# Kernel tuning notes

Hardware: AMD Instinct MI355X
Metric: run time of the kernel (lower is better)

Reference implementation:

```python
import jax, jax.numpy as jnp
import numpy as np

D, H, E, HID, TOPK = 1024, 16, 8, 2048, 2
B, L = 2, 2048

def setup_inputs() -> dict:
    key = jax.random.key(0)
    ks = jax.random.split(key, 12)
    s = 0.02
    return {
        "x": jax.random.normal(ks[0], (B, L, D), jnp.float32),
        "mask": jnp.zeros((B, L), dtype=bool),  # key_padding_mask: True = ignore
        "ln1_g": jnp.ones((D,), jnp.float32), "ln1_b": jnp.zeros((D,), jnp.float32),
        "Wqkv": jax.random.normal(ks[1], (3 * D, D), jnp.float32) * s,
        "bqkv": jnp.zeros((3 * D,), jnp.float32),
        "Wo": jax.random.normal(ks[2], (D, D), jnp.float32) * s,
        "bo": jnp.zeros((D,), jnp.float32),
        "ln2_g": jnp.ones((D,), jnp.float32), "ln2_b": jnp.zeros((D,), jnp.float32),
        "Wg": jax.random.normal(ks[3], (D, E), jnp.float32) * s,
        "bg": jnp.zeros((E,), jnp.float32),
        "W1": jax.random.normal(ks[4], (E, D, HID), jnp.float32) * s,
        "b1": jnp.zeros((E, HID), jnp.float32),
        "W2": jax.random.normal(ks[5], (E, HID, D), jnp.float32) * s,
        "b2": jnp.zeros((E, D), jnp.float32),
    }

def _layernorm(x, g, b, eps=1e-5):
    mu = x.mean(-1, keepdims=True)
    var = ((x - mu) ** 2).mean(-1, keepdims=True)
    return (x - mu) * jax.lax.rsqrt(var + eps) * g + b

def reference(x, mask, ln1_g, ln1_b, Wqkv, bqkv, Wo, bo, ln2_g, ln2_b, Wg, bg, W1, b1, W2, b2):
    b, l, d = x.shape
    dh = d // H
    # ---- pre-norm self-attention ----
    residual = x
    xn = _layernorm(x, ln1_g, ln1_b)
    qkv = xn @ Wqkv.T + bqkv                      # [B,L,3D]
    q, k, v = jnp.split(qkv, 3, axis=-1)
    q = q.reshape(b, l, H, dh).transpose(0, 2, 1, 3)  # bhld
    k = k.reshape(b, l, H, dh).transpose(0, 2, 1, 3)
    v = v.reshape(b, l, H, dh).transpose(0, 2, 1, 3)
    scores = jnp.einsum('bhqd,bhkd->bhqk', q, k) / jnp.sqrt(jnp.float32(dh))
    scores = jnp.where(mask[:, None, None, :], jnp.float32(-1e9), scores)
    attn = jax.nn.softmax(scores, axis=-1)
    ao = jnp.einsum('bhqk,bhkd->bhqd', attn, v).transpose(0, 2, 1, 3).reshape(b, l, d)
    ao = ao @ Wo.T + bo
    x = residual + ao                              # dropout is identity at eval
    # ---- pre-norm MoE FFN (top-2 softmax gating) ----
    residual = x
    xn = _layernorm(x, ln2_g, ln2_b)
    T = b * l
    xf = xn.reshape(T, d)
    probs = jax.nn.softmax(xf @ Wg + bg, axis=-1)  # [T,E]
    vals, idx = jax.lax.top_k(probs, TOPK)         # [T,K]
    wts = vals / vals.sum(-1, keepdims=True)
    # dense expert compute (reference): all experts over all tokens
    h = jax.nn.gelu(jnp.einsum('td,edh->eth', xf, W1) + b1[:, None, :], approximate=False)
    eo = jnp.einsum('eth,ehd->etd', h, W2) + b2[:, None, :]   # [E,T,D]
    sel = eo[idx, jnp.arange(T)[:, None]]          # [T,K,D]
    moe_out = (wts[..., None] * sel).sum(1).reshape(b, l, d)
    # load-balancing aux loss
    me = probs.mean(0)                             # mean gate prob per expert
    ce = jax.nn.one_hot(idx, E, dtype=probs.dtype).sum(1).mean(0)  # dispatch fraction
    moe_loss = jnp.float32(E) * jnp.sum(me * ce)
    out = residual + moe_out
    return (out, moe_loss)
```

## Files before the change

### kernel.cpp

```cpp
#include <hip/hip_runtime.h>
#include <stdint.h>

#define TOK   4096
#define DIM   1024
#define NH    16
#define DHD   64
#define NE    8
#define HIDN  2048
#define BATCH 2
#define SEQ   2048
#define BK    64

using floatx4 = __attribute__((ext_vector_type(4))) float;
using bfx8    = __attribute__((ext_vector_type(8))) __bf16;
using bfx2    = __attribute__((ext_vector_type(2))) __bf16;
using shortx8 = __attribute__((ext_vector_type(8))) short;

__device__ __forceinline__ unsigned short f2bf(float f) {
    union { __bf16 b; unsigned short u; } v;
    v.b = (__bf16)f;
    return v.u;
}

__device__ __forceinline__ float bf2f(unsigned short u) {
    union { unsigned u; float f; } v;
    v.u = (unsigned)u << 16;
    return v.f;
}

__device__ __forceinline__ unsigned pack2bf(float lo, float hi) {
    union { bfx2 v; unsigned u; } t;
    t.v[0] = (__bf16)lo;
    t.v[1] = (__bf16)hi;
    return t.u;
}

__device__ __forceinline__ float fast_gelu(float v) {
    float vc = v * (1.0f + 0.044715f * v * v);
    float e  = __builtin_amdgcn_exp2f(fminf(vc * 2.302264f, 80.0f));
    return v * e * __builtin_amdgcn_rcpf(e + 1.0f);
}

__device__ __forceinline__ floatx4 mfma16(bfx8 a, bfx8 b, floatx4 c) {
    return __builtin_amdgcn_mfma_f32_16x16x32_bf16(a, b, c, 0, 0, 0);
}

__device__ __forceinline__ void gload16(const unsigned short* g, unsigned short* l) {
    __builtin_amdgcn_global_load_lds(
        (const __attribute__((address_space(1))) unsigned int*)g,
        (__attribute__((address_space(3))) unsigned int*)l, 16, 0, 0);
}

__device__ __forceinline__ int xcd_swz(int hw, int nwg) {
    int q = nwg >> 3, r = nwg & 7;
    int xc = hw & 7, o = hw >> 3;
    return (xc < r ? xc * (q + 1) : r * (q + 1) + (xc - r) * q) + o;
}

__global__ __launch_bounds__(256) void cvt_kernel(const float* __restrict__ in,
                                                  unsigned short* __restrict__ out, int n) {
    int i = (blockIdx.x * 256 + threadIdx.x) * 4;
    if (i < n) {
        float4 v = *reinterpret_cast<const float4*>(in + i);
        out[i + 0] = f2bf(v.x);
        out[i + 1] = f2bf(v.y);
        out[i + 2] = f2bf(v.z);
        out[i + 3] = f2bf(v.w);
    }
}

__global__ __launch_bounds__(256) void transpose_cvt_kernel(const float* __restrict__ in,
                                                            unsigned short* __restrict__ out,
                                                            int R, int C) {
    __shared__ unsigned short t[64][65];
    in  += (size_t)blockIdx.z * R * C;
    out += (size_t)blockIdx.z * R * C;
    int r0 = blockIdx.y * 64, c0 = blockIdx.x * 64;
    int lr = threadIdx.x >> 4, lc = (threadIdx.x & 15) * 4;
#pragma unroll
    for (int p = 0; p < 4; p++) {
        int r = p * 16 + lr;
        float4 v = *reinterpret_cast<const float4*>(in + (size_t)(r0 + r) * C + c0 + lc);
        t[lc + 0][r] = f2bf(v.x);
        t[lc + 1][r] = f2bf(v.y);
        t[lc + 2][r] = f2bf(v.z);
        t[lc + 3][r] = f2bf(v.w);
    }
    __syncthreads();
    int c = threadIdx.x >> 2, ch = (threadIdx.x & 3) * 16;
    shortx8 o0, o1;
#pragma unroll
    for (int q = 0; q < 8; q++) { o0[q] = t[c][ch + q]; o1[q] = t[c][ch + 8 + q]; }
    unsigned short* op = out + (size_t)(c0 + c) * R + r0 + ch;
    *reinterpret_cast<shortx8*>(op) = o0;
    *reinterpret_cast<shortx8*>(op + 8) = o1;
}

__global__ __launch_bounds__(256) void kvprep_kernel(const unsigned short* __restrict__ qkv,
                                                     unsigned short* __restrict__ ktg,
                                                     unsigned short* __restrict__ vtg,
                                                     const unsigned char* __restrict__ mask,
                                                     float* __restrict__ maskf) {
    __shared__ unsigned short t[64 * 64];
    int tid = threadIdx.x;
    int s0 = blockIdx.x * 64, hd = blockIdx.y, b = blockIdx.z;
    size_t bh = (size_t)(b * NH + hd);
    if (hd == 0 && tid < 64) {
        maskf[(size_t)b * SEQ + s0 + tid] =
            mask[(size_t)b * SEQ + s0 + tid] ? -1.44269504e9f : 0.0f;
    }
#pragma unroll
    for (int i = 0; i < 2; i++) {
        int idx = i * 256 + tid;
        int sr = idx >> 3, c = idx & 7;
        shortx8 v = *reinterpret_cast<const shortx8*>(
            qkv + (size_t)(b * SEQ + s0 + sr) * 3 * DIM + DIM + hd * DHD + c * 8);
        *reinterpret_cast<shortx8*>(ktg + (bh * SEQ + s0 + sr) * DHD + c * 8) = v;
    }
#pragma unroll
    for (int i = 0; i < 2; i++) {
        int idx = i * 256 + tid;
        int sr = idx >> 3, c = idx & 7;
        shortx8 v = *reinterpret_cast<const shortx8*>(
            qkv + (size_t)(b * SEQ + s0 + sr) * 3 * DIM + 2 * DIM + hd * DHD + c * 8);
        *reinterpret_cast<shortx8*>(t + sr * 64 + ((c ^ (sr >> 3)) * 8)) = v;
    }
    __syncthreads();
#pragma unroll
    for (int i = 0; i < 2; i++) {
        int idx = i * 256 + tid;
        int d = idx >> 3, c2 = idx & 7;
        shortx8 o;
#pragma unroll
        for (int e = 0; e < 8; e++) {
            int s = c2 * 8 + e;
            o[e] = (short)t[s * 64 + (((d >> 3) ^ c2) * 8) + (d & 7)];
        }
        *reinterpret_cast<shortx8*>(vtg + (bh * DHD + d) * SEQ + s0 + c2 * 8) = o;
    }
}

__global__ __launch_bounds__(256) void ln_kernel(const float* __restrict__ x,
                                                 const float* __restrict__ g,
                                                 const float* __restrict__ b,
                                                 unsigned short* __restrict__ obf) {
    int t = blockIdx.x;
    int tid = threadIdx.x;
    const float* xr = x + (size_t)t * DIM;
    float4 v = *reinterpret_cast<const float4*>(xr + tid * 4);
    float s  = v.x + v.y + v.z + v.w;
    float s2 = v.x * v.x + v.y * v.y + v.z * v.z + v.w * v.w;
    for (int o = 32; o > 0; o >>= 1) {
        s  += __shfl_down(s,  o, 64);
        s2 += __shfl_down(s2, o, 64);
    }
    __shared__ float red[10];
    int lane = tid & 63, w = tid >> 6;
    if (lane == 0) { red[w] = s; red[4 + w] = s2; }
    __syncthreads();
    if (tid == 0) {
        float ts = red[0] + red[1] + red[2] + red[3];
        float t2 = red[4] + red[5] + red[6] + red[7];
        float mu = ts * (1.0f / DIM);
        float var = t2 * (1.0f / DIM) - mu * mu;
        red[8] = mu;
        red[9] = rsqrtf(var + 1e-5f);
    }
    __syncthreads();
    float mu = red[8], rstd = red[9];
    float4 gv = *reinterpret_cast<const float4*>(g + tid * 4);
    float4 bv = *reinterpret_cast<const float4*>(b + tid * 4);
    size_t o = (size_t)t * DIM + tid * 4;
    obf[o + 0] = f2bf((v.x - mu) * rstd * gv.x + bv.x);
    obf[o + 1] = f2bf((v.y - mu) * rstd * gv.y + bv.y);
    obf[o + 2] = f2bf((v.z - mu) * rstd * gv.z + bv.z);
    obf[o + 3] = f2bf((v.w - mu) * rstd * gv.w + bv.w);
}

template <int EPI, bool GATHER>
__global__ __launch_bounds__(256) void gemm_kernel(const unsigned short* __restrict__ A,
                                                   const unsigned short* __restrict__ Bt,
                                                   void* __restrict__ C,
                                                   const float* __restrict__ bias,
                                                   const float* __restrict__ resid,
                                                   const int* __restrict__ cnt,
                                                   const int* __restrict__ goff,
                                                   const int* __restrict__ gtok,
                                                   int M, int N, int K) {
    int gx = gridDim.x, gy = gridDim.y;
    int nwg = gx * gy * (int)gridDim.z;
    int hw = ((int)blockIdx.z * gy + (int)blockIdx.y) * gx + (int)blockIdx.x;
    int virt = xcd_swz(hw, nwg);
    int bx = virt % gx;
    int tmp = virt / gx;
    int by = tmp % gy;
    int e = tmp / gy;

    int Me = cnt ? cnt[e] : M;
    int brow = by * 128;
    if (brow >= Me) return;
    int bcol = bx * 128;
    int go = goff ? goff[e] : 0;
    const unsigned short* Be = Bt + (size_t)e * N * K;
    const float* biasp = bias + (size_t)e * N;

    __shared__ unsigned short As[128 * BK];
    __shared__ unsigned short Bs[128 * BK];

    int tid = threadIdx.x, lane = tid & 63, w = tid >> 6;
    int wr = w >> 1, wc = w & 1;
    int cg = lane >> 4, cl = lane & 15;

    const unsigned short* aga[4];
    const unsigned short* bga[4];
    unsigned short* asb = As + w * 2048;
    unsigned short* bsb = Bs + w * 2048;
#pragma unroll
    for (int i = 0; i < 4; i++) {
        int s = w * 256 + i * 64 + lane;
        int row = s >> 3;
        int c = (s & 7) ^ (row & 7);
        int gr = brow + row;
        if (gr >= Me) gr = Me - 1;
        long ar;
        if (GATHER) ar = gtok[go + gr];
        else if (cnt) ar = go + gr;
        else ar = gr;
        aga[i] = A + ar * (long)K + c * 8;
        bga[i] = Be + (size_t)(bcol + row) * K + c * 8;
    }

    floatx4 acc[4][4];
#pragma unroll
    for (int m = 0; m < 4; m++)
#pragma unroll
        for (int n = 0; n < 4; n++) acc[m][n] = (floatx4){0.f, 0.f, 0.f, 0.f};

    for (int kt = 0; kt < K; kt += BK) {
#pragma unroll
        for (int i = 0; i < 4; i++) {
            gload16(aga[i], asb + i * 512);
            gload16(bga[i], bsb + i * 512);
            aga[i] += BK;
            bga[i] += BK;
        }
        __syncthreads();
#pragma unroll
        for (int ks = 0; ks < 2; ks++) {
            bfx8 af[4], bf[4];
#pragma unroll
            for (int m = 0; m < 4; m++) {
                int row = wr * 64 + m * 16 + cl;
                af[m] = *reinterpret_cast<const bfx8*>(
                    As + row * BK + (((ks * 4 + cg) ^ (row & 7)) << 3));
            }
#pragma unroll
            for (int n = 0; n < 4; n++) {
                int row = wc * 64 + n * 16 + cl;
                bf[n] = *reinterpret_cast<const bfx8*>(
                    Bs + row * BK + (((ks * 4 + cg) ^ (row & 7)) << 3));
            }
#pragma unroll
            for (int m = 0; m < 4; m++)
#pragma unroll
                for (int n = 0; n < 4; n++) acc[m][n] = mfma16(af[m], bf[n], acc[m][n]);
        }
        __syncthreads();
    }

#pragma unroll
    for (int m = 0; m < 4; m++) {
#pragma unroll
        for (int j = 0; j < 4; j++) {
            int r = brow + wr * 64 + m * 16 + cg * 4 + j;
            if (r >= Me) continue;
#pragma unroll
            for (int n = 0; n < 4; n++) {
                int col = bcol + wc * 64 + n * 16 + cl;
                float v = acc[m][n][j] + biasp[col];
                if (EPI == 0) {
                    ((unsigned short*)C)[(size_t)r * N + col] = f2bf(v);
                } else if (EPI == 1) {
                    size_t o = (size_t)r * N + col;
                    ((float*)C)[o] = v + resid[o];
                } else if (EPI == 2) {
                    ((unsigned short*)C)[(size_t)(go + r) * N + col] = f2bf(fast_gelu(v));
                } else {
                    ((unsigned short*)C)[(size_t)(go + r) * N + col] = f2bf(v);
                }
            }
        }
    }
}

__global__ __launch_bounds__(512, 2) void attn_kernel(const unsigned short* __restrict__ qkv,
                                                      const unsigned short* __restrict__ ktg,
                                                      const unsigned short* __restrict__ vtg,
                                                      const float* __restrict__ maskf,
                                                      unsigned short* __restrict__ ao) {
    __shared__ unsigned short Ks[2][64 * 64];
    __shared__ unsigned short Vs[2][64 * 64];
    __shared__ unsigned short Ps[8][16 * 72];

    int tid = threadIdx.x, lane = tid & 63, w = tid >> 6;
    int cg = lane >> 4, cl = lane & 15;
    int qb = blockIdx.x * 128, hd = blockIdx.y, b = blockIdx.z;
    size_t bh = (size_t)(b * NH + hd);
    const float SC2 = 0.125f * 1.44269504f;

    int tq = qb + w * 16 + cl;
    const unsigned short* qrow = qkv + (size_t)(b * SEQ + tq) * 3 * DIM + hd * DHD;
    bfx8 aq0 = *reinterpret_cast<const bfx8*>(qrow + cg * 8);
    bfx8 aq1 = *reinterpret_cast<const bfx8*>(qrow + 32 + cg * 8);

    int srow8 = lane >> 3, schunk = lane & 7;
    int csrc = schunk ^ srow8;
    const unsigned short* kptr = ktg + (bh * SEQ + w * 8 + srow8) * DHD + csrc * 8;
    const unsigned short* vptr = vtg + (bh * DHD + w * 8 + srow8) * SEQ + csrc * 8;
    const float* mrowf = maskf + (size_t)b * SEQ;
    unsigned short* psw = &Ps[w][0];
    int sw0 = (cg ^ (cl & 7)) << 3;

    floatx4 accO[4];
#pragma unroll
    for (int dt = 0; dt < 4; dt++) accO[dt] = (floatx4){0.f, 0.f, 0.f, 0.f};
    float m0 = -3.0e38f, l0 = 0.f;

    gload16(kptr, &Ks[0][tid * 8]);
    gload16(vptr, &Vs[0][tid * 8]);
    __syncthreads();

    int cur = 0;
    for (int t = 0; t < SEQ / 64; t++) {
        if (t < SEQ / 64 - 1) {
            size_t nkt = (size_t)(t + 1) * 64;
            int nb = cur ^ 1;
            gload16(kptr + nkt * DHD, &Ks[nb][tid * 8]);
            gload16(vptr + nkt, &Vs[nb][tid * 8]);
        }
        const unsigned short* ksb = &Ks[cur][0];
        const unsigned short* vsb = &Vs[cur][0];
        int kt = t * 64;

        float4 mk[4];
#pragma unroll
        for (int nt = 0; nt < 4; nt++)
            mk[nt] = *reinterpret_cast<const float4*>(mrowf + kt + nt * 16 + cg * 4);

        floatx4 accS[4];
#pragma unroll
        for (int nt = 0; nt < 4; nt++) accS[nt] = (floatx4){0.f, 0.f, 0.f, 0.f};
        __builtin_amdgcn_s_setprio(1);
#pragma unroll
        for (int nt = 0; nt < 4; nt++) {
            const unsigned short* kr = ksb + (nt * 16 + cl) * 64;
            bfx8 k0 = *reinterpret_cast<const bfx8*>(kr + sw0);
            bfx8 k1 = *reinterpret_cast<const bfx8*>(kr + (sw0 ^ 32));
            accS[nt] = mfma16(k0, aq0, accS[nt]);
            accS[nt] = mfma16(k1, aq1, accS[nt]);
        }
        __builtin_amdgcn_s_setprio(0);

        float s[4][4];
        float pm[4];
#pragma unroll
        for (int nt = 0; nt < 4; nt++) {
            s[nt][0] = fmaf(accS[nt][0], SC2, mk[nt].x);
            s[nt][1] = fmaf(accS[nt][1], SC2, mk[nt].y);
            s[nt][2] = fmaf(accS[nt][2], SC2, mk[nt].z);
            s[nt][3] = fmaf(accS[nt][3], SC2, mk[nt].w);
            pm[nt] = fmaxf(fmaxf(s[nt][0], s[nt][1]), fmaxf(s[nt][2], s[nt][3]));
        }
        float tmax = fmaxf(fmaxf(pm[0], pm[1]), fmaxf(pm[2], pm[3]));
        if (!__all(tmax - m0 <= 11.5f)) {
            tmax = fmaxf(tmax, __shfl_xor(tmax, 16, 64));
            tmax = fmaxf(tmax, __shfl_xor(tmax, 32, 64));
            float mn = fmaxf(m0, tmax);
            float al = __builtin_amdgcn_exp2f(m0 - mn);
            m0 = mn;
            l0 *= al;
#pragma unroll
            for (int dt = 0; dt < 4; dt++) accO[dt] *= al;
        }

        float rs = 0.f;
#pragma unroll
        for (int nt = 0; nt < 4; nt++) {
            float p0 = __builtin_amdgcn_exp2f(s[nt][0] - m0);
            float p1 = __builtin_amdgcn_exp2f(s[nt][1] - m0);
            float p2 = __builtin_amdgcn_exp2f(s[nt][2] - m0);
            float p3 = __builtin_amdgcn_exp2f(s[nt][3] - m0);
            rs += (p0 + p1) + (p2 + p3);
            uint2 u;
            u.x = pack2bf(p0, p1);
            u.y = pack2bf(p2, p3);
            *reinterpret_cast<uint2*>(psw + cl * 72 + nt * 16 + cg * 4) = u;
        }
        rs += __shfl_xor(rs, 16, 64);
        rs += __shfl_xor(rs, 32, 64);
        l0 += rs;

        bfx8 pf0 = *reinterpret_cast<const bfx8*>(psw + cl * 72 + cg * 8);
        bfx8 pf1 = *reinterpret_cast<const bfx8*>(psw + cl * 72 + 32 + cg * 8);
        __builtin_amdgcn_s_setprio(1);
#pragma unroll
        for (int dt = 0; dt < 4; dt++) {
            const unsigned short* vr = vsb + (dt * 16 + cl) * 64;
            bfx8 v0 = *reinterpret_cast<const bfx8*>(vr + sw0);
            bfx8 v1 = *reinterpret_cast<const bfx8*>(vr + (sw0 ^ 32));
            accO[dt] = mfma16(v0, pf0, accO[dt]);
            accO[dt] = mfma16(v1, pf1, accO[dt]);
        }
        __builtin_amdgcn_s_setprio(0);
        __syncthreads();
        cur ^= 1;
    }

    float rl = 1.0f / l0;
    unsigned short* aorow = ao + (size_t)(b * SEQ + qb + w * 16 + cl) * DIM + hd * DHD;
#pragma unroll
    for (int dt = 0; dt < 4; dt++) {
        uint2 u;
        u.x = pack2bf(accO[dt][0] * rl, accO[dt][1] * rl);
        u.y = pack2bf(accO[dt][2] * rl, accO[dt][3] * rl);
        *reinterpret_cast<uint2*>(aorow + dt * 16 + cg * 4) = u;
    }
}

__global__ __launch_bounds__(256) void gate_kernel(const float* __restrict__ x2,
                                                   const float* __restrict__ lng,
                                                   const float* __restrict__ lnb,
                                                   const float* __restrict__ Wg,
                                                   const float* __restrict__ bg,
                                                   unsigned short* __restrict__ xn2b,
                                                   int* __restrict__ idx,
                                                   float* __restrict__ wts,
                                                   float* __restrict__ me_part) {
    __shared__ float bme[8];
    if (threadIdx.x < 8) bme[threadIdx.x] = 0.f;
    __syncthreads();
    int w = threadIdx.x >> 6, lane = threadIdx.x & 63;
    int t = blockIdx.x * 4 + w;
    const float* xr = x2 + (size_t)t * DIM + lane * 16;
    float4 xv[4];
    float s = 0.f, s2 = 0.f;
#pragma unroll
    for (int q = 0; q < 4; q++) {
        xv[q] = *reinterpret_cast<const float4*>(xr + q * 4);
        s  += xv[q].x + xv[q].y + xv[q].z + xv[q].w;
        s2 += xv[q].x * xv[q].x + xv[q].y * xv[q].y + xv[q].z * xv[q].z + xv[q].w * xv[q].w;
    }
    for (int o = 32; o > 0; o >>= 1) {
        s  += __shfl_xor(s,  o, 64);
        s2 += __shfl_xor(s2, o, 64);
    }
    float mu = s * (1.0f / DIM);
    float rstd = rsqrtf(s2 * (1.0f / DIM) - mu * mu + 1e-5f);
    float acc[8];
#pragma unroll
    for (int e = 0; e < 8; e++) acc[e] = 0.f;
    unsigned short ob[16];
#pragma unroll
    for (int q = 0; q < 4; q++) {
        float4 gv = *reinterpret_cast<const float4*>(lng + lane * 16 + q * 4);
        float4 bv = *reinterpret_cast<const float4*>(lnb + lane * 16 + q * 4);
        float xn0 = (xv[q].x - mu) * rstd * gv.x + bv.x;
        float xn1 = (xv[q].y - mu) * rstd * gv.y + bv.y;
        float xn2 = (xv[q].z - mu) * rstd * gv.z + bv.z;
        float xn3 = (xv[q].w - mu) * rstd * gv.w + bv.w;
        ob[q * 4 + 0] = f2bf(xn0);
        ob[q * 4 + 1] = f2bf(xn1);
        ob[q * 4 + 2] = f2bf(xn2);
        ob[q * 4 + 3] = f2bf(xn3);
        const float* wr = Wg + (size_t)(lane * 16 + q * 4) * 8;
#pragma unroll
        for (int e = 0; e < 8; e++) acc[e] += xn0 * wr[e];
#pragma unroll
        for (int e = 0; e < 8; e++) acc[e] += xn1 * wr[8 + e];
#pragma unroll
        for (int e = 0; e < 8; e++) acc[e] += xn2 * wr[16 + e];
#pragma unroll
        for (int e = 0; e < 8; e++) acc[e] += xn3 * wr[24 + e];
    }
    unsigned short* op = xn2b + (size_t)t * DIM + lane * 16;
    *reinterpret_cast<shortx8*>(op)     = *reinterpret_cast<shortx8*>(&ob[0]);
    *reinterpret_cast<shortx8*>(op + 8) = *reinterpret_cast<shortx8*>(&ob[8]);
    for (int o = 32; o > 0; o >>= 1)
#pragma unroll
        for (int e = 0; e < 8; e++) acc[e] += __shfl_xor(acc[e], o, 64);
    if (lane == 0) {
        float p[8];
        float mx = -3e38f;
#pragma unroll
        for (int e = 0; e < 8; e++) { acc[e] += bg[e]; mx = fmaxf(mx, acc[e]); }
        float se = 0.f;
#pragma unroll
        for (int e = 0; e < 8; e++) { p[e] = expf(acc[e] - mx); se += p[e]; }
#pragma unroll
        for (int e = 0; e < 8; e++) p[e] /= se;
        int i0 = 0; float v0 = p[0];
#pragma unroll
        for (int e = 1; e < 8; e++) if (p[e] > v0) { v0 = p[e]; i0 = e; }
        int i1 = -1; float v1 = -3e38f;
#pragma unroll
        for (int e = 0; e < 8; e++) if (e != i0 && p[e] > v1) { v1 = p[e]; i1 = e; }
        float sw = v0 + v1;
        idx[t * 2]     = i0;
        idx[t * 2 + 1] = i1;
        wts[t * 2]     = v0 / sw;
        wts[t * 2 + 1] = v1 / sw;
#pragma unroll
        for (int e = 0; e < 8; e++) atomicAdd(&bme[e], p[e]);
    }
    __syncthreads();
    if (threadIdx.x < 8) me_part[(size_t)blockIdx.x * 8 + threadIdx.x] = bme[threadIdx.x];
}

__global__ __launch_bounds__(256) void route1_kernel(const int* __restrict__ idx,
                                                     int* __restrict__ cnt,
                                                     int* __restrict__ posl) {
    __shared__ int lh[8];
    __shared__ int gb[8];
    int tid = threadIdx.x;
    int t = blockIdx.x * 256 + tid;
    if (tid < 8) lh[tid] = 0;
    __syncthreads();
    int i0 = idx[t * 2], i1 = idx[t * 2 + 1];
    int r0 = atomicAdd(&lh[i0], 1);
    int r1 = atomicAdd(&lh[i1], 1);
    __syncthreads();
    if (tid < 8) gb[tid] = atomicAdd(&cnt[tid], lh[tid]);
    __syncthreads();
    posl[t * 2]     = gb[i0] + r0;
    posl[t * 2 + 1] = gb[i1] + r1;
}

__global__ void prefix_kernel(const int* __restrict__ cnt, int* __restrict__ goff) {
    if (threadIdx.x == 0) {
        int s = 0;
        for (int e = 0; e < 8; e++) { goff[e] = s; s += cnt[e]; }
        goff[8] = s;
    }
}

__global__ __launch_bounds__(256) void route2_kernel(const int* __restrict__ idx,
                                                     const int* __restrict__ goff,
                                                     const int* __restrict__ posl,
                                                     int* __restrict__ gtok,
                                                     int* __restrict__ tpos) {
    int t = blockIdx.x * 256 + threadIdx.x;
#pragma unroll
    for (int j = 0; j < 2; j++) {
        int e = idx[t * 2 + j];
        int p = goff[e] + posl[t * 2 + j];
        gtok[p] = t;
        tpos[t * 2 + j] = p;
    }
}

__global__ __launch_bounds__(256) void combine_kernel(const float* __restrict__ x2,
                                                      const unsigned short* __restrict__ eo,
                                                      const float* __restrict__ wts,
                                                      const int* __restrict__ tpos,
                                                      float* __restrict__ out) {
    int t = blockIdx.x;
    int c = threadIdx.x * 4;
    float w0 = wts[t * 2], w1 = wts[t * 2 + 1];
    int p0 = tpos[t * 2], p1 = tpos[t * 2 + 1];
    float4 r = *reinterpret_cast<const float4*>(x2 + (size_t)t * DIM + c);
    ushort4 a4 = *reinterpret_cast<const ushort4*>(eo + (size_t)p0 * DIM + c);
    ushort4 b4 = *reinterpret_cast<const ushort4*>(eo + (size_t)p1 * DIM + c);
    float4 o;
    o.x = r.x + w0 * bf2f(a4.x) + w1 * bf2f(b4.x);
    o.y = r.y + w0 * bf2f(a4.y) + w1 * bf2f(b4.y);
    o.z = r.z + w0 * bf2f(a4.z) + w1 * bf2f(b4.z);
    o.w = r.w + w0 * bf2f(a4.w) + w1 * bf2f(b4.w);
    *reinterpret_cast<float4*>(out + (size_t)t * DIM + c) = o;
}

__global__ __launch_bounds__(256) void loss_kernel(const float* __restrict__ me_part,
                                                   const int* __restrict__ cnt,
                                                   float* __restrict__ out) {
    __shared__ float red[256];
    int tid = threadIdx.x;
    int e = tid & 7, part = tid >> 3;
    float s = 0.f;
    for (int b = part; b < 1024; b += 32) s += me_part[(size_t)b * 8 + e];
    red[tid] = s;
    __syncthreads();
    if (tid < 64) {
        float v = red[tid] + red[tid + 64] + red[tid + 128] + red[tid + 192];
        red[tid] = v;
    }
    __syncthreads();
    if (tid < 8) {
        float v = red[tid] + red[tid + 8] + red[tid + 16] + red[tid + 24] +
                  red[tid + 32] + red[tid + 40] + red[tid + 48] + red[tid + 56];
        red[tid] = v;
    }
    __syncthreads();
    if (tid == 0) {
        float s2 = 0.f;
        for (int ee = 0; ee < 8; ee++)
            s2 += (red[ee] / 4096.0f) * ((float)cnt[ee] / 4096.0f);
        out[(size_t)TOK * DIM] = 8.0f * s2;
    }
}

extern "C" void kernel_launch(void* const* d_in, const int* in_sizes, int n_in,
                              void* d_out, int out_size, void* d_ws, size_t ws_size,
                              hipStream_t stream) {
    const float* x    = (const float*)d_in[0];
    const unsigned char* mask = (const unsigned char*)d_in[1];
    const float* ln1g = (const float*)d_in[2];
    const float* ln1b = (const float*)d_in[3];
    const float* Wqkv = (const float*)d_in[4];
    const float* bqkv = (const float*)d_in[5];
    const float* Wo   = (const float*)d_in[6];
    const float* bo   = (const float*)d_in[7];
    const float* ln2g = (const float*)d_in[8];
    const float* ln2b = (const float*)d_in[9];
    const float* Wg   = (const float*)d_in[10];
    const float* bg   = (const float*)d_in[11];
    const float* W1   = (const float*)d_in[12];
    const float* b1   = (const float*)d_in[13];
    const float* W2   = (const float*)d_in[14];
    const float* b2   = (const float*)d_in[15];
    float* out = (float*)d_out;

    char* ws = (char*)d_ws;
    int*   cnt  = (int*)(ws + 0);
    int*   goff = (int*)(ws + 128);
    size_t off = 1024;
    auto alloc = [&](size_t bytes) -> void* {
        void* p = ws + off;
        off += (bytes + 255) & ~(size_t)255;
        return p;
    };
    const size_t SZ_QKVB = (size_t)TOK * 3 * DIM * 2;
    const size_t SZ_HB   = (size_t)2 * TOK * HIDN * 2;
    char* R1 = (char*)alloc(SZ_HB > SZ_QKVB ? SZ_HB : SZ_QKVB);
    const size_t SZ_R2 = (size_t)2 * TOK * DIM * 2 + (size_t)3 * DIM * DIM * 2 +
                         (size_t)DIM * DIM * 2;
    char* R2 = (char*)alloc(SZ_R2);
    unsigned short* qkvb  = (unsigned short*)R1;
    unsigned short* hb    = (unsigned short*)R1;
    unsigned short* eo16  = (unsigned short*)R2;
    unsigned short* xn1   = (unsigned short*)R2;
    unsigned short* aob   = (unsigned short*)(R2 + (size_t)TOK * DIM * 2);
    unsigned short* wqkvb = (unsigned short*)(R2 + (size_t)2 * TOK * DIM * 2);
    unsigned short* wob   = (unsigned short*)(R2 + (size_t)2 * TOK * DIM * 2 +
                                              (size_t)3 * DIM * DIM * 2);
    float*          x2    = (float*)alloc((size_t)TOK * DIM * 4);
    unsigned short* xn2b  = (unsigned short*)alloc((size_t)TOK * DIM * 2);
    unsigned short* w1t   = (unsigned short*)alloc((size_t)NE * DIM * HIDN * 2);
    unsigned short* w2t   = (unsigned short*)alloc((size_t)NE * DIM * HIDN * 2);
    unsigned short* ktg   = (unsigned short*)alloc((size_t)BATCH * NH * SEQ * DHD * 2);
    unsigned short* vtg   = (unsigned short*)alloc((size_t)BATCH * NH * DHD * SEQ * 2);
    float*          maskf = (float*)alloc((size_t)BATCH * SEQ * 4);
    float*          mep   = (float*)alloc((size_t)1024 * 8 * 4);
    int*            idxp  = (int*)alloc((size_t)TOK * 2 * 4);
    float*          wtsp  = (float*)alloc((size_t)TOK * 2 * 4);
    int*            posl  = (int*)alloc((size_t)TOK * 2 * 4);
    int*            gtok  = (int*)alloc((size_t)2 * TOK * 4);
    int*            tpos  = (int*)alloc((size_t)TOK * 2 * 4);

    hipMemsetAsync(ws, 0, 256, stream);

    cvt_kernel<<<3 * DIM * DIM / 1024, 256, 0, stream>>>(Wqkv, wqkvb, 3 * DIM * DIM);
    cvt_kernel<<<DIM * DIM / 1024, 256, 0, stream>>>(Wo, wob, DIM * DIM);
    transpose_cvt_kernel<<<dim3(HIDN / 64, DIM / 64, NE), 256, 0, stream>>>(W1, w1t, DIM, HIDN);
    transpose_cvt_kernel<<<dim3(DIM / 64, HIDN / 64, NE), 256, 0, stream>>>(W2, w2t, HIDN, DIM);

    ln_kernel<<<TOK, 256, 0, stream>>>(x, ln1g, ln1b, xn1);

    gemm_kernel<0, false><<<dim3(24, 32, 1), 256, 0, stream>>>(
        xn1, wqkvb, qkvb, bqkv, nullptr, nullptr, nullptr, nullptr, TOK, 3 * DIM, DIM);

    kvprep_kernel<<<dim3(SEQ / 64, NH, BATCH), 256, 0, stream>>>(qkvb, ktg, vtg, mask, maskf);

    attn_kernel<<<dim3(SEQ / 128, NH, BATCH), 512, 0, stream>>>(qkvb, ktg, vtg, maskf, aob);

    gemm_kernel<1, false><<<dim3(8, 32, 1), 256, 0, stream>>>(
        aob, wob, x2, bo, x, nullptr, nullptr, nullptr, TOK, DIM, DIM);

    gate_kernel<<<TOK / 4, 256, 0, stream>>>(x2, ln2g, ln2b, Wg, bg, xn2b,
                                             idxp, wtsp, mep);
    route1_kernel<<<TOK / 256, 256, 0, stream>>>(idxp, cnt, posl);
    prefix_kernel<<<1, 64, 0, stream>>>(cnt, goff);
    route2_kernel<<<TOK / 256, 256, 0, stream>>>(idxp, goff, posl, gtok, tpos);

    gemm_kernel<2, true><<<dim3(16, 32, 8), 256, 0, stream>>>(
        xn2b, w1t, hb, b1, nullptr, cnt, goff, gtok, TOK, HIDN, DIM);

    gemm_kernel<3, false><<<dim3(8, 32, 8), 256, 0, stream>>>(
        hb, w2t, eo16, b2, nullptr, cnt, goff, nullptr, TOK, DIM, HIDN);

    combine_kernel<<<TOK, 256, 0, stream>>>(x2, eo16, wtsp, tpos, out);
    loss_kernel<<<1, 256, 0, stream>>>(mep, cnt, out);
}
```

Before: 337.4 us.

## Use 256-row, 512-thread tiles for MoE expert GEMMs and XCD-swizzle attention grid

New measurement: 392.0 us. 16.2% more time.

```diff
diff --git a/kernel.cpp b/kernel.cpp
--- a/kernel.cpp
+++ b/kernel.cpp
@@ -293,6 +293,133 @@
     }
 }
 
+template <int EPI, bool GATHER, int BN>
+__global__ __launch_bounds__(512, 2) void gemm256_kernel(const unsigned short* __restrict__ A,
+                                                         const unsigned short* __restrict__ Bt,
+                                                         void* __restrict__ C,
+                                                         const float* __restrict__ bias,
+                                                         const int* __restrict__ cnt,
+                                                         const int* __restrict__ goff,
+                                                         const int* __restrict__ gtok,
+                                                         int M, int N, int K) {
+    constexpr int NREP = BN / 64;
+    constexpr int RB   = BN / 64;
+    int gx = gridDim.x, gy = gridDim.y;
+    int nwg = gx * gy * (int)gridDim.z;
+    int hw = ((int)blockIdx.z * gy + (int)blockIdx.y) * gx + (int)blockIdx.x;
+    int virt = xcd_swz(hw, nwg);
+    int bx = virt % gx;
+    int tmp = virt / gx;
+    int by = tmp % gy;
+    int e = tmp / gy;
+
+    int Me = cnt[e];
+    int brow = by * 256;
+    if (brow >= Me) return;
+    int bcol = bx * BN;
+    int go = goff[e];
+    const unsigned short* Be = Bt + (size_t)e * N * K;
+    const float* biasp = bias + (size_t)e * N;
+
+    __shared__ unsigned short As[2][256 * BK];
+    __shared__ unsigned short Bs[2][BN * BK];
+
+    int tid = threadIdx.x, lane = tid & 63, w = tid >> 6;
+    int wr = w >> 2, wc = w & 3;
+    int cg = lane >> 4, cl = lane & 15;
+
+    const unsigned short* aga[4];
+    const unsigned short* bga[RB];
+#pragma unroll
+    for (int r = 0; r < 4; r++) {
+        int s = r * 512 + tid;
+        int row = s >> 3;
+        int c = (s & 7) ^ (row & 7);
+        int gr = brow + row;
+        if (gr >= Me) gr = Me - 1;
+        long ar;
+        if (GATHER) ar = gtok[go + gr];
+        else ar = go + gr;
+        aga[r] = A + ar * (long)K + c * 8;
+    }
+#pragma unroll
+    for (int r = 0; r < RB; r++) {
+        int s = r * 512 + tid;
+        int row = s >> 3;
+        int c = (s & 7) ^ (row & 7);
+        bga[r] = Be + (size_t)(bcol + row) * K + c * 8;
+    }
+
+    floatx4 acc[8][NREP];
+#pragma unroll
+    for (int m = 0; m < 8; m++)
+#pragma unroll
+        for (int n = 0; n < NREP; n++) acc[m][n] = (floatx4){0.f, 0.f, 0.f, 0.f};
+
+#pragma unroll
+    for (int r = 0; r < 4; r++) { gload16(aga[r], &As[0][(r * 512 + tid) * 8]); aga[r] += BK; }
+#pragma unroll
+    for (int r = 0; r < RB; r++) { gload16(bga[r], &Bs[0][(r * 512 + tid) * 8]); bga[r] += BK; }
+    __syncthreads();
+
+    int nt = K / BK;
+    int cur = 0;
+    for (int t = 0; t < nt; t++) {
+        if (t + 1 < nt) {
+            int nb = cur ^ 1;
+#pragma unroll
+            for (int r = 0; r < 4; r++) { gload16(aga[r], &As[nb][(r * 512 + tid) * 8]); aga[r] += BK; }
+#pragma unroll
+            for (int r = 0; r < RB; r++) { gload16(bga[r], &Bs[nb][(r * 512 + tid) * 8]); bga[r] += BK; }
+        }
+        const unsigned short* asb = &As[cur][0];
+        const unsigned short* bsb = &Bs[cur][0];
+#pragma unroll
+        for (int ks = 0; ks < 2; ks++) {
+            bfx8 af[8], bf[NREP];
+#pragma unroll
+            for (int m = 0; m < 8; m++) {
+                int row = wr * 128 + m * 16 + cl;
+                af[m] = *reinterpret_cast<const bfx8*>(
+                    asb + row * BK + (((ks * 4 + cg) ^ (row & 7)) << 3));
+            }
+#pragma unroll
+            for (int n = 0; n < NREP; n++) {
+                int row = wc * (BN / 4) + n * 16 + cl;
+                bf[n] = *reinterpret_cast<const bfx8*>(
+                    bsb + row * BK + (((ks * 4 + cg) ^ (row & 7)) << 3));
+            }
+            __builtin_amdgcn_s_setprio(1);
+#pragma unroll
+            for (int m = 0; m < 8; m++)
+#pragma unroll
+                for (int n = 0; n < NREP; n++) acc[m][n] = mfma16(af[m], bf[n], acc[m][n]);
+            __builtin_amdgcn_s_setprio(0);
+        }
+        __syncthreads();
+        cur ^= 1;
+    }
+
+#pragma unroll
+    for (int m = 0; m < 8; m++) {
+#pragma unroll
+        for (int j = 0; j < 4; j++) {
+            int r = brow + wr * 128 + m * 16 + cg * 4 + j;
+            if (r >= Me) continue;
+#pragma unroll
+            for (int n = 0; n < NREP; n++) {
+                int col = bcol + wc * (BN / 4) + n * 16 + cl;
+                float v = acc[m][n][j] + biasp[col];
+                if (EPI == 2) {
+                    ((unsigned short*)C)[(size_t)(go + r) * N + col] = f2bf(fast_gelu(v));
+                } else {
+                    ((unsigned short*)C)[(size_t)(go + r) * N + col] = f2bf(v);
+                }
+            }
+        }
+    }
+}
+
 __global__ __launch_bounds__(512, 2) void attn_kernel(const unsigned short* __restrict__ qkv,
                                                       const unsigned short* __restrict__ ktg,
                                                       const unsigned short* __restrict__ vtg,
@@ -304,7 +431,15 @@
 
     int tid = threadIdx.x, lane = tid & 63, w = tid >> 6;
     int cg = lane >> 4, cl = lane & 15;
-    int qb = blockIdx.x * 128, hd = blockIdx.y, b = blockIdx.z;
+    int gx = gridDim.x, gy = gridDim.y;
+    int nwg = gx * gy * (int)gridDim.z;
+    int hw = ((int)blockIdx.z * gy + (int)blockIdx.y) * gx + (int)blockIdx.x;
+    int virt = xcd_swz(hw, nwg);
+    int qx = virt % gx;
+    int tmp = virt / gx;
+    int hd = tmp % gy;
+    int b = tmp / gy;
+    int qb = qx * 128;
     size_t bh = (size_t)(b * NH + hd);
     const float SC2 = 0.125f * 1.44269504f;
 
@@ -690,11 +825,11 @@
     prefix_kernel<<<1, 64, 0, stream>>>(cnt, goff);
     route2_kernel<<<TOK / 256, 256, 0, stream>>>(idxp, goff, posl, gtok, tpos);
 
-    gemm_kernel<2, true><<<dim3(16, 32, 8), 256, 0, stream>>>(
-        xn2b, w1t, hb, b1, nullptr, cnt, goff, gtok, TOK, HIDN, DIM);
-
-    gemm_kernel<3, false><<<dim3(8, 32, 8), 256, 0, stream>>>(
-        hb, w2t, eo16, b2, nullptr, cnt, goff, nullptr, TOK, DIM, HIDN);
+    gemm256_kernel<2, true, 256><<<dim3(HIDN / 256, 16, 8), 512, 0, stream>>>(
+        xn2b, w1t, hb, b1, cnt, goff, gtok, TOK, HIDN, DIM);
+
+    gemm256_kernel<3, false, 128><<<dim3(DIM / 128, 16, 8), 512, 0, stream>>>(
+        hb, w2t, eo16, b2, cnt, goff, nullptr, TOK, DIM, HIDN);
 
     combine_kernel<<<TOK, 256, 0, stream>>>(x2, eo16, wtsp, tpos, out);
     loss_kernel<<<1, 256, 0, stream>>>(mep, cnt, out);
```
